# Kernel tuning notes

Hardware: AMD Instinct MI355X
Metric: run time of the kernel (lower is better)

## Reference

```python
import jax, jax.numpy as jnp
import numpy as np


def color_bin(x, n_bins):
    """Per-image 3D color histogram over n_bins**3 flat bins.
    x: [B, 3, H, W] float in ~[-1, 1]. Returns [B, n_bins**3] float32.
    """
    B, C, H, W = x.shape
    n_tot = n_bins ** 3
    # torch color_bins: i*(2/n_bins) - 1 for i in 1..n_bins-1
    boundaries = jnp.arange(1, n_bins, dtype=jnp.float32) * (2.0 / n_bins) - 1.0
    # torch.bucketize(right=False) == searchsorted side='left'
    idx = jnp.searchsorted(boundaries, x.reshape(B, C, H * W), side='left')  # [B,3,HW] int
    scale = jnp.array([1, n_bins, n_bins ** 2], dtype=idx.dtype)
    flat = jnp.einsum('bcp,c->bp', idx, scale)  # [B, HW], values in [0, n_tot)
    # torch.histc(bins, n_tot, min=0, max=n_tot-1) on exact integers == bincount
    hist = jax.vmap(lambda f: jnp.bincount(f, length=n_tot))(flat)
    return hist.astype(jnp.float32) / (H * W)


def setup_inputs() -> dict:
    key = jax.random.key(0)
    k1, k2 = jax.random.split(key)
    inp = jax.random.normal(k1, (8, 3, 1024, 1024), dtype=jnp.float32)
    style = jax.random.normal(k2, (1, 3, 1024, 1024), dtype=jnp.float32)
    return {"input": inp, "style_image": style, "n_bins": 16}


def reference(input, style_image, n_bins):
    # target histogram from the style image (detached in torch; ints anyway)
    target = color_bin(style_image, n_bins).squeeze(0)  # [n_tot]
    cols = color_bin(input, n_bins)                     # [B, n_tot]
    # F.l1_loss(cols, target.repeat(B, 1)) with mean reduction
    loss = jnp.mean(jnp.abs(cols - target[None, :]))
    return loss
```

## Files before the change

kernel.cpp:

```cpp
#include <hip/hip_runtime.h>

#define HW      (1024 * 1024)
#define HW4     (HW / 4)
#define NBINS   4096
#define NIMG    9
#define BPI     64
#define THREADS 256
#define F4_PER_BLOCK (HW4 / BPI)

__device__ __forceinline__ int bin16(float x) {
    int lo = 0;
    if (0.0f < x) lo = 8;
    if ((float)(lo + 4) * 0.125f - 1.0f < x) lo += 4;
    if ((float)(lo + 2) * 0.125f - 1.0f < x) lo += 2;
    if ((float)(lo + 1) * 0.125f - 1.0f < x) lo += 1;
    return lo;
}

__device__ __forceinline__ int bin3(float r, float g, float b) {
    return bin16(r) + 16 * bin16(g) + 256 * bin16(b);
}

__global__ __launch_bounds__(THREADS) void hist_kernel(
        const float* __restrict__ input,
        const float* __restrict__ style,
        int* __restrict__ ghist) {
    __shared__ int lh[NBINS];
    const int img = blockIdx.y;
    const float* base = (img < 8) ? (input + (size_t)img * 3 * HW) : style;

    for (int i = threadIdx.x; i < NBINS; i += THREADS) lh[i] = 0;
    __syncthreads();

    const float4* c0 = (const float4*)(base);
    const float4* c1 = (const float4*)(base + HW);
    const float4* c2 = (const float4*)(base + 2 * HW);
    const int start = blockIdx.x * F4_PER_BLOCK;

    for (int j = threadIdx.x; j < F4_PER_BLOCK; j += THREADS) {
        const int p = start + j;
        float4 r = c0[p];
        float4 g = c1[p];
        float4 b = c2[p];
        atomicAdd(&lh[bin3(r.x, g.x, b.x)], 1);
        atomicAdd(&lh[bin3(r.y, g.y, b.y)], 1);
        atomicAdd(&lh[bin3(r.z, g.z, b.z)], 1);
        atomicAdd(&lh[bin3(r.w, g.w, b.w)], 1);
    }
    __syncthreads();

    int* gh = ghist + (size_t)img * NBINS;
    for (int i = threadIdx.x; i < NBINS; i += THREADS) {
        const int v = lh[i];
        if (v) atomicAdd(&gh[i], v);
    }
}

__global__ __launch_bounds__(1024) void loss_kernel(
        const int* __restrict__ ghist, float* __restrict__ out) {
    __shared__ long long part[16];
    const int* tgt = ghist + 8 * NBINS;
    long long acc = 0;
    for (int e = threadIdx.x; e < 8 * NBINS; e += 1024) {
        const int b = e >> 12;
        const int i = e & (NBINS - 1);
        const int d = ghist[b * NBINS + i] - tgt[i];
        acc += (d < 0) ? (long long)(-d) : (long long)d;
    }
    for (int off = 32; off; off >>= 1) acc += __shfl_down(acc, off, 64);
    const int lane = threadIdx.x & 63;
    const int wv   = threadIdx.x >> 6;
    if (lane == 0) part[wv] = acc;
    __syncthreads();
    if (wv == 0) {
        long long t = (lane < 16) ? part[lane] : 0;
        for (int off = 8; off; off >>= 1) t += __shfl_down(t, off, 64);
        if (lane == 0) {
            out[0] = (float)((double)t / (1048576.0 * 32768.0));
        }
    }
}

extern "C" void kernel_launch(void* const* d_in, const int* in_sizes, int n_in,
                              void* d_out, int out_size, void* d_ws, size_t ws_size,
                              hipStream_t stream) {
    const float* input = (const float*)d_in[0];
    const float* style = (const float*)d_in[1];
    int* ghist = (int*)d_ws;

    hipMemsetAsync(d_ws, 0, NIMG * NBINS * sizeof(int), stream);

    dim3 grid(BPI, NIMG);
    hipLaunchKernelGGL(hist_kernel, grid, dim3(THREADS), 0, stream,
                       input, style, ghist);
    hipLaunchKernelGGL(loss_kernel, dim3(1), dim3(1024), 0, stream,
                       ghist, (float*)d_out);
}
```

Baseline: 175.7 us.

## Replace global atomic merge with per-block partial histograms and reduction kernel

Each histogram block now writes its full shared-memory histogram to a private slice of workspace instead of atomically adding into a global histogram, and a new reduce kernel sums the per-block slices. The memset is removed, the block count per image is doubled, and the inner loop loads two float4 triples per iteration for more memory parallelism. The aim is to remove global atomic contention and the memset launch. In exchange it adds an extra kernel launch and about 19 MB of partial-histogram traffic.

```diff
diff --git a/kernel.cpp b/kernel.cpp
--- a/kernel.cpp
+++ b/kernel.cpp
@@ -4,7 +4,7 @@
 #define HW4     (HW / 4)
 #define NBINS   4096
 #define NIMG    9
-#define BPI     64
+#define BPI     128
 #define THREADS 256
 #define F4_PER_BLOCK (HW4 / BPI)
 
@@ -21,12 +21,20 @@
     return bin16(r) + 16 * bin16(g) + 256 * bin16(b);
 }
 
+__device__ __forceinline__ void acc4(int* lh, float4 r, float4 g, float4 b) {
+    atomicAdd(&lh[bin3(r.x, g.x, b.x)], 1);
+    atomicAdd(&lh[bin3(r.y, g.y, b.y)], 1);
+    atomicAdd(&lh[bin3(r.z, g.z, b.z)], 1);
+    atomicAdd(&lh[bin3(r.w, g.w, b.w)], 1);
+}
+
 __global__ __launch_bounds__(THREADS) void hist_kernel(
         const float* __restrict__ input,
         const float* __restrict__ style,
-        int* __restrict__ ghist) {
+        int* __restrict__ part) {
     __shared__ int lh[NBINS];
     const int img = blockIdx.y;
+    const int blk = blockIdx.x;
     const float* base = (img < 8) ? (input + (size_t)img * 3 * HW) : style;
 
     for (int i = threadIdx.x; i < NBINS; i += THREADS) lh[i] = 0;
@@ -35,48 +43,56 @@
     const float4* c0 = (const float4*)(base);
     const float4* c1 = (const float4*)(base + HW);
     const float4* c2 = (const float4*)(base + 2 * HW);
-    const int start = blockIdx.x * F4_PER_BLOCK;
+    const int start = blk * F4_PER_BLOCK;
 
-    for (int j = threadIdx.x; j < F4_PER_BLOCK; j += THREADS) {
-        const int p = start + j;
-        float4 r = c0[p];
-        float4 g = c1[p];
-        float4 b = c2[p];
-        atomicAdd(&lh[bin3(r.x, g.x, b.x)], 1);
-        atomicAdd(&lh[bin3(r.y, g.y, b.y)], 1);
-        atomicAdd(&lh[bin3(r.z, g.z, b.z)], 1);
-        atomicAdd(&lh[bin3(r.w, g.w, b.w)], 1);
+    for (int j = threadIdx.x; j < F4_PER_BLOCK; j += 2 * THREADS) {
+        const int p0 = start + j;
+        const int p1 = p0 + THREADS;
+        float4 r0 = c0[p0], g0 = c1[p0], b0 = c2[p0];
+        float4 r1 = c0[p1], g1 = c1[p1], b1 = c2[p1];
+        acc4(lh, r0, g0, b0);
+        acc4(lh, r1, g1, b1);
     }
     __syncthreads();
 
-    int* gh = ghist + (size_t)img * NBINS;
-    for (int i = threadIdx.x; i < NBINS; i += THREADS) {
-        const int v = lh[i];
-        if (v) atomicAdd(&gh[i], v);
-    }
+    int4* dst = (int4*)(part + ((size_t)img * BPI + blk) * NBINS);
+    const int4* src = (const int4*)lh;
+    for (int i = threadIdx.x; i < NBINS / 4; i += THREADS) dst[i] = src[i];
+}
+
+__global__ __launch_bounds__(THREADS) void reduce_kernel(
+        const int* __restrict__ part,
+        int* __restrict__ H) {
+    const int img = blockIdx.y;
+    const int bin = blockIdx.x * THREADS + threadIdx.x;
+    const int* p = part + (size_t)img * BPI * NBINS + bin;
+    int sum = 0;
+#pragma unroll 8
+    for (int b = 0; b < BPI; ++b) sum += p[(size_t)b * NBINS];
+    H[img * NBINS + bin] = sum;
 }
 
 __global__ __launch_bounds__(1024) void loss_kernel(
-        const int* __restrict__ ghist, float* __restrict__ out) {
-    __shared__ long long part[16];
-    const int* tgt = ghist + 8 * NBINS;
+        const int* __restrict__ H, float* __restrict__ out) {
+    __shared__ long long partsum[16];
+    const int* tgt = H + 8 * NBINS;
     long long acc = 0;
     for (int e = threadIdx.x; e < 8 * NBINS; e += 1024) {
         const int b = e >> 12;
         const int i = e & (NBINS - 1);
-        const int d = ghist[b * NBINS + i] - tgt[i];
+        const int d = H[b * NBINS + i] - tgt[i];
         acc += (d < 0) ? (long long)(-d) : (long long)d;
     }
     for (int off = 32; off; off >>= 1) acc += __shfl_down(acc, off, 64);
     const int lane = threadIdx.x & 63;
     const int wv   = threadIdx.x >> 6;
-    if (lane == 0) part[wv] = acc;
+    if (lane == 0) partsum[wv] = acc;
     __syncthreads();
     if (wv == 0) {
-        long long t = (lane < 16) ? part[lane] : 0;
+        long long t = (lane < 16) ? partsum[lane] : 0;
         for (int off = 8; off; off >>= 1) t += __shfl_down(t, off, 64);
         if (lane == 0) {
-            out[0] = (float)((double)t / (1048576.0 * 32768.0));
+            out[0] = (float)((double)t / 34359738368.0);
         }
     }
 }
@@ -86,13 +102,13 @@
                               hipStream_t stream) {
     const float* input = (const float*)d_in[0];
     const float* style = (const float*)d_in[1];
-    int* ghist = (int*)d_ws;
+    int* part = (int*)d_ws;
+    int* H    = part + (size_t)NIMG * BPI * NBINS;
 
-    hipMemsetAsync(d_ws, 0, NIMG * NBINS * sizeof(int), stream);
-
-    dim3 grid(BPI, NIMG);
-    hipLaunchKernelGGL(hist_kernel, grid, dim3(THREADS), 0, stream,
-                       input, style, ghist);
+    hipLaunchKernelGGL(hist_kernel, dim3(BPI, NIMG), dim3(THREADS), 0, stream,
+                       input, style, part);
+    hipLaunchKernelGGL(reduce_kernel, dim3(NBINS / THREADS, NIMG), dim3(THREADS),
+                       0, stream, part, H);
     hipLaunchKernelGGL(loss_kernel, dim3(1), dim3(1024), 0, stream,
-                       ghist, (float*)d_out);
+                       H, (float*)d_out);
 }
```

New measurement: 182.1 us. 1.04x slower.
